# Kernel optimization log

Hardware: AMD Instinct MI355X
Metric: run time of the kernel (lower is better)

The kernel has to match this reference:

```python
import jax, jax.numpy as jnp
import numpy as np

SIM_COEFF = 25.0
COV_COEFF = 1.0
N, D = 32768, 512


def setup_inputs() -> dict:
    key = jax.random.key(0)
    k1, k2, k3 = jax.random.split(key, 3)
    z_a = jax.random.normal(k1, (N, D), dtype=jnp.float32)
    z_b = jax.random.normal(k2, (N, D), dtype=jnp.float32)
    # torch.randperm(N): values in [0, N) even though `combined` has 2N rows,
    # so both halves are drawn from z_a only (faithful to the original code).
    perm = jax.random.permutation(k3, N).astype(jnp.int32)
    return {"z_a": z_a, "z_b": z_b, "perm": perm}


def reference(z_a, z_b, perm):
    n, d = z_a.shape
    half = n // 2
    # repr (invariance) loss: MSE with mean reduction
    repr_loss = jnp.mean((z_a - z_b) ** 2)
    # combined has 2N rows but perm values < N -> selects rows of z_a
    combined = jnp.concatenate([z_a, z_b], axis=0)  # [2N, D]
    z1 = combined[perm[:half]]   # [N//2, D]
    z2 = combined[perm[half:]]   # [N - N//2, D]
    denom = jnp.float32(half - 1)  # original divides BOTH by N//2 - 1
    cov_z1 = (z1.T @ z1) / denom   # [D, D], replaces the per-sample outer-product loop
    cov_z2 = (z2.T @ z2) / denom   # [D, D]
    I = jnp.eye(d, dtype=z_a.dtype)
    cov_diff = (cov_z1 - I) @ (cov_z2 - I)
    cov_loss = jnp.sqrt(jnp.sum(cov_diff ** 2))  # Frobenius norm
    return SIM_COEFF * repr_loss + COV_COEFF * cov_loss
```

## Files before the change

kernel.cpp:

```cpp
#include <hip/hip_runtime.h>
#include <math.h>

typedef unsigned short u16;
typedef __attribute__((ext_vector_type(8))) short s16x8;
typedef __attribute__((ext_vector_type(4))) float f32x4;

#define NROWS 32768
#define DDIM 512
#define HALF 16384
#define KB 64
#define CSLICE 4
#define NSLICE 32
#define NSLOG2 5

__device__ __forceinline__ u16 f2bf(float f) {
  unsigned int u = __float_as_uint(f);
  unsigned int rounding = 0x7FFFu + ((u >> 16) & 1u);
  u += rounding;
  return (u16)(u >> 16);
}

__device__ __forceinline__ float bf2f(u16 h) {
  return __uint_as_float(((unsigned)h) << 16);
}

__device__ __forceinline__ float block_reduce(float v) {
  #pragma unroll
  for (int o = 32; o > 0; o >>= 1) v += __shfl_down(v, o);
  __shared__ float red[4];
  int w = threadIdx.x >> 6;
  if ((threadIdx.x & 63) == 0) red[w] = v;
  __syncthreads();
  return red[0] + red[1] + red[2] + red[3];
}

__global__ void inv_kernel(const int* __restrict__ perm, int* __restrict__ inv) {
  int i = blockIdx.x * 256 + threadIdx.x;
  inv[perm[i]] = i;
}

__device__ __forceinline__ float chunk_proc(float4 a0, float4 a1, float4 b0, float4 b1,
                                            int r, int c8, u16* z1, u16* z2) {
  uint4 o;
  o.x = (unsigned)f2bf(a0.x) | ((unsigned)f2bf(a0.y) << 16);
  o.y = (unsigned)f2bf(a0.z) | ((unsigned)f2bf(a0.w) << 16);
  o.z = (unsigned)f2bf(a1.x) | ((unsigned)f2bf(a1.y) << 16);
  o.w = (unsigned)f2bf(a1.z) | ((unsigned)f2bf(a1.w) << 16);
  u16* dst = (r < HALF) ? (z1 + (size_t)r * DDIM + c8) : (z2 + (size_t)(r - HALF) * DDIM + c8);
  *reinterpret_cast<uint4*>(dst) = o;
  float dx = a0.x - b0.x, dy = a0.y - b0.y, dz = a0.z - b0.z, dw = a0.w - b0.w;
  float ex = a1.x - b1.x, ey = a1.y - b1.y, ez = a1.z - b1.z, ew = a1.w - b1.w;
  return dx*dx + dy*dy + dz*dz + dw*dw + ex*ex + ey*ey + ez*ez + ew*ew;
}

__global__ __launch_bounds__(256) void scatter_repr_kernel(
    const float* __restrict__ za, const float* __restrict__ zb, const int* __restrict__ inv,
    u16* __restrict__ z1, u16* __restrict__ z2, float* __restrict__ psums) {
  int t = threadIdx.x;
  float acc = 0.0f;
  #pragma unroll
  for (int i = 0; i < 4; ++i) {
    int chunk = (i * 2048 + blockIdx.x) * 256 + t;
    int row = chunk >> 6;
    int c8 = (chunk & 63) << 3;
    const float4* pa = reinterpret_cast<const float4*>(za + (size_t)row * DDIM + c8);
    const float4* pb = reinterpret_cast<const float4*>(zb + (size_t)row * DDIM + c8);
    float4 a0 = pa[0], a1 = pa[1];
    float4 b0 = pb[0], b1 = pb[1];
    int r = inv[row];
    acc += chunk_proc(a0, a1, b0, b1, r, c8, z1, z2);
  }
  float tot = block_reduce(acc);
  if (t == 0) psums[blockIdx.x] = tot;
}

__device__ __forceinline__ int swz(int col) { return (((col >> 3) + col) & 7) << 3; }

__device__ __forceinline__ void store8(u16* lds, int c0, int kp, uint4 v0, uint4 v1) {
  const ushort* h0 = reinterpret_cast<const ushort*>(&v0);
  const ushort* h1 = reinterpret_cast<const ushort*>(&v1);
  #pragma unroll
  for (int j = 0; j < 8; ++j) {
    int col = c0 + j;
    unsigned w = (unsigned)h0[j] | ((unsigned)h1[j] << 16);
    *reinterpret_cast<unsigned*>(lds + col * KB + ((kp ^ swz(col)))) = w;
  }
}

__global__ __launch_bounds__(256) void gram_kernel(const u16* __restrict__ z1,
                                                   const u16* __restrict__ z2,
                                                   u16* __restrict__ parts) {
  int b = blockIdx.x;
  int mat = b & 1;
  int rest = b >> 1;
  int slice = rest & (NSLICE - 1);
  int tile = rest >> NSLOG2;
  int bi, bj;
  if (tile < 4)      { bi = 0; bj = tile; }
  else if (tile < 7) { bi = 1; bj = tile - 3; }
  else if (tile < 9) { bi = 2; bj = tile - 5; }
  else               { bi = 3; bj = 3; }
  int ti = bi * 128, tj = bj * 128;
  const u16* Z = mat ? z2 : z1;
  bool dual = (ti != tj);
  u16* P = parts + ((size_t)(mat * NSLICE + slice)) * (DDIM * DDIM);

  __shared__ u16 ldsA[128 * KB];
  __shared__ u16 ldsB[128 * KB];
  const u16* ldsBp = dual ? ldsB : ldsA;

  int t = threadIdx.x;
  int lane = t & 63;
  int wave = t >> 6;
  int wrow = (wave >> 1) * 64;
  int wcol = (wave & 1) * 64;
  int g = lane >> 4;
  int c = lane & 15;
  int h = lane >> 4;
  int c0 = (lane & 15) << 3;
  int kp0 = 8 * wave + 2 * h;

  f32x4 acc[4][4];
  #pragma unroll
  for (int m = 0; m < 4; ++m)
    #pragma unroll
    for (int n = 0; n < 4; ++n)
      #pragma unroll
      for (int r = 0; r < 4; ++r) acc[m][n][r] = 0.0f;

  uint4 xa0, xa1, xa2, xa3, xb0, xb1, xb2, xb3;
  uint4 ya0, ya1, ya2, ya3, yb0, yb1, yb2, yb3;

#define GLOAD(p, kkv) { \
    const u16* s0 = Z + (size_t)((kkv) + kp0) * DDIM; \
    const u16* s1 = Z + (size_t)((kkv) + kp0 + 32) * DDIM; \
    p##a0 = *reinterpret_cast<const uint4*>(s0 + ti + c0); \
    p##a1 = *reinterpret_cast<const uint4*>(s0 + DDIM + ti + c0); \
    p##a2 = *reinterpret_cast<const uint4*>(s1 + ti + c0); \
    p##a3 = *reinterpret_cast<const uint4*>(s1 + DDIM + ti + c0); \
    if (dual) { \
      p##b0 = *reinterpret_cast<const uint4*>(s0 + tj + c0); \
      p##b1 = *reinterpret_cast<const uint4*>(s0 + DDIM + tj + c0); \
      p##b2 = *reinterpret_cast<const uint4*>(s1 + tj + c0); \
      p##b3 = *reinterpret_cast<const uint4*>(s1 + DDIM + tj + c0); \
    } }

#define GSTORE(p) { \
    store8(ldsA, c0, kp0, p##a0, p##a1); \
    store8(ldsA, c0, kp0 + 32, p##a2, p##a3); \
    if (dual) { \
      store8(ldsB, c0, kp0, p##b0, p##b1); \
      store8(ldsB, c0, kp0 + 32, p##b2, p##b3); \
    } }

#define COMPUTE() { \
    _Pragma("unroll") \
    for (int ks = 0; ks < KB; ks += 32) { \
      s16x8 afr[4], bfr[4]; \
      _Pragma("unroll") \
      for (int m = 0; m < 4; ++m) { \
        int colA = wrow + m * 16 + c; \
        afr[m] = *reinterpret_cast<const s16x8*>(ldsA + colA * KB + ((ks + 8 * g) ^ swz(colA))); \
        int colB = wcol + m * 16 + c; \
        bfr[m] = *reinterpret_cast<const s16x8*>(ldsBp + colB * KB + ((ks + 8 * g) ^ swz(colB))); \
      } \
      _Pragma("unroll") \
      for (int m = 0; m < 4; ++m) \
        _Pragma("unroll") \
        for (int n = 0; n < 4; ++n) \
          acc[m][n] = __builtin_amdgcn_mfma_f32_16x16x32_bf16(afr[m], bfr[n], acc[m][n], 0, 0, 0); \
    } }

  const int kspan = HALF >> NSLOG2;
  const int k0 = slice * kspan;
  GLOAD(x, k0);
  for (int kk = k0; kk < k0 + kspan; kk += 2 * KB) {
    __syncthreads();
    GSTORE(x);
    __syncthreads();
    GLOAD(y, kk + KB);
    COMPUTE();
    __syncthreads();
    GSTORE(y);
    __syncthreads();
    if (kk + 2 * KB < k0 + kspan) GLOAD(x, kk + 2 * KB);
    COMPUTE();
  }
#undef GLOAD
#undef GSTORE
#undef COMPUTE

  #pragma unroll
  for (int m = 0; m < 4; ++m)
    #pragma unroll
    for (int n = 0; n < 4; ++n)
      #pragma unroll
      for (int r = 0; r < 4; ++r) {
        int orow = ti + wrow + m * 16 + 4 * g + r;
        int ocol = tj + wcol + n * 16 + c;
        P[orow * DDIM + ocol] = f2bf(acc[m][n][r]);
      }
}

__global__ void reduce_parts_kernel(const u16* __restrict__ parts, float* __restrict__ cov) {
  int idx = blockIdx.x * 256 + threadIdx.x;
  int mat = (idx >= 40960) ? 1 : 0;
  int tl = idx - mat * 40960;
  int region = tl >> 12;
  int o = tl & 4095;
  int bi, bj;
  if (region < 4)      { bi = 0; bj = region; }
  else if (region < 7) { bi = 1; bj = region - 3; }
  else if (region < 9) { bi = 2; bj = region - 5; }
  else                 { bi = 3; bj = 3; }
  int r = bi * 128 + (o >> 5);
  int cc = bj * 128 + ((o & 31) << 2);
  const u16* base = parts + (size_t)mat * NSLICE * (DDIM * DDIM);
  float sx = 0.f, sy = 0.f, sz = 0.f, sw = 0.f;
  #pragma unroll 4
  for (int j = 0; j < NSLICE; ++j) {
    ushort4 v = *reinterpret_cast<const ushort4*>(base + (size_t)j * (DDIM * DDIM) + r * DDIM + cc);
    sx += bf2f(v.x); sy += bf2f(v.y); sz += bf2f(v.z); sw += bf2f(v.w);
  }
  const float inv = 1.0f / 16383.0f;
  sx *= inv; sy *= inv; sz *= inv; sw *= inv;
  float* cv = cov + (size_t)mat * (DDIM * DDIM);
  float4 ov; ov.x = sx; ov.y = sy; ov.z = sz; ov.w = sw;
  *reinterpret_cast<float4*>(cv + r * DDIM + cc) = ov;
  if (bi != bj) {
    cv[(cc + 0) * DDIM + r] = sx;
    cv[(cc + 1) * DDIM + r] = sy;
    cv[(cc + 2) * DDIM + r] = sz;
    cv[(cc + 3) * DDIM + r] = sw;
  }
}

__global__ __launch_bounds__(256) void covdiff_part_kernel(const float* __restrict__ cov,
                                                           float* __restrict__ pcov) {
  int bid = blockIdx.x;
  int bx = bid & 15, by = (bid >> 4) & 15, sl = bid >> 8;
  int r0 = by * 32, c0 = bx * 32, ks = sl * 128;
  const float* c1 = cov;
  const float* c2 = cov + DDIM * DDIM;
  __shared__ float ldsA[32 * 132];
  __shared__ float ldsB[128 * 33];
  int t = threadIdx.x;
  #pragma unroll
  for (int j = 0; j < 4; ++j) {
    int f4 = t + 256 * j;
    int row = f4 >> 5;
    int k4 = (f4 & 31) << 2;
    float4 v = *reinterpret_cast<const float4*>(c1 + (size_t)(r0 + row) * DDIM + ks + k4);
    int gr = r0 + row;
    if (gr == ks + k4 + 0) v.x -= 1.f;
    if (gr == ks + k4 + 1) v.y -= 1.f;
    if (gr == ks + k4 + 2) v.z -= 1.f;
    if (gr == ks + k4 + 3) v.w -= 1.f;
    *reinterpret_cast<float4*>(&ldsA[row * 132 + k4]) = v;
  }
  {
    int c = t & 31;
    int kb = t >> 5;
    #pragma unroll
    for (int j = 0; j < 16; ++j) {
      int k = kb + 8 * j;
      float v = c2[(size_t)(ks + k) * DDIM + c0 + c];
      if (ks + k == c0 + c) v -= 1.f;
      ldsB[k * 33 + c] = v;
    }
  }
  __syncthreads();
  int col = t & 31;
  int ty = t >> 5;
  float e0 = 0.f, e1 = 0.f, e2 = 0.f, e3 = 0.f;
  #pragma unroll 4
  for (int k = 0; k < 128; ++k) {
    float bv = ldsB[k * 33 + col];
    e0 = fmaf(ldsA[(ty * 4 + 0) * 132 + k], bv, e0);
    e1 = fmaf(ldsA[(ty * 4 + 1) * 132 + k], bv, e1);
    e2 = fmaf(ldsA[(ty * 4 + 2) * 132 + k], bv, e2);
    e3 = fmaf(ldsA[(ty * 4 + 3) * 132 + k], bv, e3);
  }
  float* P = pcov + (size_t)sl * (DDIM * DDIM);
  P[(r0 + ty * 4 + 0) * DDIM + c0 + col] = e0;
  P[(r0 + ty * 4 + 1) * DDIM + c0 + col] = e1;
  P[(r0 + ty * 4 + 2) * DDIM + c0 + col] = e2;
  P[(r0 + ty * 4 + 3) * DDIM + c0 + col] = e3;
}

__global__ void covred_kernel(const float* __restrict__ pcov, float* __restrict__ psums2) {
  int idx = blockIdx.x * 256 + threadIdx.x;
  float sx = 0.f, sy = 0.f, sz = 0.f, sw = 0.f;
  #pragma unroll
  for (int j = 0; j < CSLICE; ++j) {
    float4 v = reinterpret_cast<const float4*>(pcov)[idx + j * 65536];
    sx += v.x; sy += v.y; sz += v.z; sw += v.w;
  }
  float q = sx * sx + sy * sy + sz * sz + sw * sw;
  float tot = block_reduce(q);
  if (threadIdx.x == 0) psums2[blockIdx.x] = tot;
}

__global__ void finalize_kernel(const float* __restrict__ psums,
                                const float* __restrict__ psums2,
                                float* __restrict__ out) {
  int t = threadIdx.x;
  float a = 0.f;
  #pragma unroll
  for (int j = 0; j < 8; ++j) a += psums[t + 256 * j];
  float b = psums2[t];
  float ta = block_reduce(a);
  __syncthreads();
  float tb = block_reduce(b);
  if (t == 0) out[0] = 25.0f * (ta / 16777216.0f) + sqrtf(tb);
}

extern "C" void kernel_launch(void* const* d_in, const int* in_sizes, int n_in,
                              void* d_out, int out_size, void* d_ws, size_t ws_size,
                              hipStream_t stream) {
  const float* za = (const float*)d_in[0];
  const float* zb = (const float*)d_in[1];
  const int* perm = (const int*)d_in[2];
  float* out = (float*)d_out;
  char* ws = (char*)d_ws;

  float* psums = (float*)ws;
  float* psums2 = (float*)(ws + 8192);
  size_t off = 16384;
  u16* parts = (u16*)(ws + off);
  off += (size_t)2 * NSLICE * DDIM * DDIM * 2;
  float* cov = (float*)(ws + off);
  off += (size_t)2 * DDIM * DDIM * 4;
  u16* z1 = (u16*)(ws + off);
  u16* z2 = z1 + (size_t)HALF * DDIM;
  float* pcov = (float*)z1;
  off += (size_t)2 * HALF * DDIM * 2;
  int* inv = (int*)(ws + off);

  inv_kernel<<<NROWS / 256, 256, 0, stream>>>(perm, inv);
  scatter_repr_kernel<<<2048, 256, 0, stream>>>(za, zb, inv, z1, z2, psums);
  gram_kernel<<<2 * 10 * NSLICE, 256, 0, stream>>>(z1, z2, parts);
  reduce_parts_kernel<<<320, 256, 0, stream>>>(parts, cov);
  covdiff_part_kernel<<<16 * 16 * CSLICE, 256, 0, stream>>>(cov, pcov);
  covred_kernel<<<256, 256, 0, stream>>>(pcov, psums2);
  finalize_kernel<<<1, 256, 0, stream>>>(psums, psums2, out);
}
```

Measured before the change: 78.96 us.

## Accumulate Gram split-K partials with fp32 atomics instead of bf16 slice buffers

The Gram kernel now adds its per-slice partial results straight into a zeroed fp32 buffer with atomicAdd, instead of writing 32 bf16 partial matrices that a later kernel had to read back and sum. The reduce kernel becomes a simple scale-and-mirror fixup, and a memset is added to clear the accumulator. This removes about 32 MB of partial writes and reads, at the cost of atomic contention on 32 slices per element and an extra memset. The scatter kernel also gets twice as many blocks, each doing half the work, with the final reduction widened to match.

```diff
diff --git a/kernel.cpp b/kernel.cpp
--- a/kernel.cpp
+++ b/kernel.cpp
@@ -18,10 +18,6 @@
   unsigned int rounding = 0x7FFFu + ((u >> 16) & 1u);
   u += rounding;
   return (u16)(u >> 16);
-}
-
-__device__ __forceinline__ float bf2f(u16 h) {
-  return __uint_as_float(((unsigned)h) << 16);
 }
 
 __device__ __forceinline__ float block_reduce(float v) {
@@ -59,8 +55,8 @@
   int t = threadIdx.x;
   float acc = 0.0f;
   #pragma unroll
-  for (int i = 0; i < 4; ++i) {
-    int chunk = (i * 2048 + blockIdx.x) * 256 + t;
+  for (int i = 0; i < 2; ++i) {
+    int chunk = (i * 4096 + blockIdx.x) * 256 + t;
     int row = chunk >> 6;
     int c8 = (chunk & 63) << 3;
     const float4* pa = reinterpret_cast<const float4*>(za + (size_t)row * DDIM + c8);
@@ -89,7 +85,7 @@
 
 __global__ __launch_bounds__(256) void gram_kernel(const u16* __restrict__ z1,
                                                    const u16* __restrict__ z2,
-                                                   u16* __restrict__ parts) {
+                                                   float* __restrict__ rawG) {
   int b = blockIdx.x;
   int mat = b & 1;
   int rest = b >> 1;
@@ -103,7 +99,7 @@
   int ti = bi * 128, tj = bj * 128;
   const u16* Z = mat ? z2 : z1;
   bool dual = (ti != tj);
-  u16* P = parts + ((size_t)(mat * NSLICE + slice)) * (DDIM * DDIM);
+  float* G = rawG + (size_t)mat * (DDIM * DDIM);
 
   __shared__ u16 ldsA[128 * KB];
   __shared__ u16 ldsB[128 * KB];
@@ -198,11 +194,11 @@
       for (int r = 0; r < 4; ++r) {
         int orow = ti + wrow + m * 16 + 4 * g + r;
         int ocol = tj + wcol + n * 16 + c;
-        P[orow * DDIM + ocol] = f2bf(acc[m][n][r]);
+        atomicAdd(&G[orow * DDIM + ocol], acc[m][n][r]);
       }
 }
 
-__global__ void reduce_parts_kernel(const u16* __restrict__ parts, float* __restrict__ cov) {
+__global__ void fixup_kernel(const float* __restrict__ rawG, float* __restrict__ cov) {
   int idx = blockIdx.x * 256 + threadIdx.x;
   int mat = (idx >= 40960) ? 1 : 0;
   int tl = idx - mat * 40960;
@@ -215,23 +211,17 @@
   else                 { bi = 3; bj = 3; }
   int r = bi * 128 + (o >> 5);
   int cc = bj * 128 + ((o & 31) << 2);
-  const u16* base = parts + (size_t)mat * NSLICE * (DDIM * DDIM);
-  float sx = 0.f, sy = 0.f, sz = 0.f, sw = 0.f;
-  #pragma unroll 4
-  for (int j = 0; j < NSLICE; ++j) {
-    ushort4 v = *reinterpret_cast<const ushort4*>(base + (size_t)j * (DDIM * DDIM) + r * DDIM + cc);
-    sx += bf2f(v.x); sy += bf2f(v.y); sz += bf2f(v.z); sw += bf2f(v.w);
-  }
+  size_t pos = (size_t)r * DDIM + cc;
+  float4 v = *reinterpret_cast<const float4*>(rawG + (size_t)mat * (DDIM * DDIM) + pos);
   const float inv = 1.0f / 16383.0f;
-  sx *= inv; sy *= inv; sz *= inv; sw *= inv;
+  v.x *= inv; v.y *= inv; v.z *= inv; v.w *= inv;
   float* cv = cov + (size_t)mat * (DDIM * DDIM);
-  float4 ov; ov.x = sx; ov.y = sy; ov.z = sz; ov.w = sw;
-  *reinterpret_cast<float4*>(cv + r * DDIM + cc) = ov;
+  *reinterpret_cast<float4*>(cv + pos) = v;
   if (bi != bj) {
-    cv[(cc + 0) * DDIM + r] = sx;
-    cv[(cc + 1) * DDIM + r] = sy;
-    cv[(cc + 2) * DDIM + r] = sz;
-    cv[(cc + 3) * DDIM + r] = sw;
+    cv[(cc + 0) * DDIM + r] = v.x;
+    cv[(cc + 1) * DDIM + r] = v.y;
+    cv[(cc + 2) * DDIM + r] = v.z;
+    cv[(cc + 3) * DDIM + r] = v.w;
   }
 }
 
@@ -307,7 +297,7 @@
   int t = threadIdx.x;
   float a = 0.f;
   #pragma unroll
-  for (int j = 0; j < 8; ++j) a += psums[t + 256 * j];
+  for (int j = 0; j < 16; ++j) a += psums[t + 256 * j];
   float b = psums2[t];
   float ta = block_reduce(a);
   __syncthreads();
@@ -325,10 +315,11 @@
   char* ws = (char*)d_ws;
 
   float* psums = (float*)ws;
-  float* psums2 = (float*)(ws + 8192);
-  size_t off = 16384;
-  u16* parts = (u16*)(ws + off);
-  off += (size_t)2 * NSLICE * DDIM * DDIM * 2;
+  float* psums2 = (float*)(ws + 16384);
+  size_t off = 20480;
+  float* rawG = (float*)(ws + off);
+  size_t rawBytes = (size_t)2 * DDIM * DDIM * 4;
+  off += rawBytes;
   float* cov = (float*)(ws + off);
   off += (size_t)2 * DDIM * DDIM * 4;
   u16* z1 = (u16*)(ws + off);
@@ -337,10 +328,11 @@
   off += (size_t)2 * HALF * DDIM * 2;
   int* inv = (int*)(ws + off);
 
+  (void)hipMemsetAsync(rawG, 0, rawBytes, stream);
   inv_kernel<<<NROWS / 256, 256, 0, stream>>>(perm, inv);
-  scatter_repr_kernel<<<2048, 256, 0, stream>>>(za, zb, inv, z1, z2, psums);
-  gram_kernel<<<2 * 10 * NSLICE, 256, 0, stream>>>(z1, z2, parts);
-  reduce_parts_kernel<<<320, 256, 0, stream>>>(parts, cov);
+  scatter_repr_kernel<<<4096, 256, 0, stream>>>(za, zb, inv, z1, z2, psums);
+  gram_kernel<<<2 * 10 * NSLICE, 256, 0, stream>>>(z1, z2, rawG);
+  fixup_kernel<<<320, 256, 0, stream>>>(rawG, cov);
   covdiff_part_kernel<<<16 * 16 * CSLICE, 256, 0, stream>>>(cov, pcov);
   covred_kernel<<<256, 256, 0, stream>>>(pcov, psums2);
   finalize_kernel<<<1, 256, 0, stream>>>(psums, psums2, out);
```

Result: slower. 106.2 us (+34.4%).

## Fuse permutation gather and bf16 conversion into the Gram kernel

Applied to the files above, without the earlier changes.

Drops the inverse-permutation and scatter kernels that wrote permuted bf16 copies of z_a into the workspace. The Gram kernel now stages its 512-row slice of perm in LDS, gathers fp32 rows of z_a directly, and packs them to bf16 before storing to LDS. The repr loss becomes a plain streaming kernel over z_a and z_b. This removes a full write and re-read of the bf16 intermediate plus one launch, at the cost of the Gram kernel reading fp32 rows by scattered index and holding twice as many prefetch registers.

```diff
diff --git a/kernel.cpp b/kernel.cpp
--- a/kernel.cpp
+++ b/kernel.cpp
@@ -13,11 +13,11 @@
 #define NSLICE 32
 #define NSLOG2 5
 
-__device__ __forceinline__ u16 f2bf(float f) {
+__device__ __forceinline__ unsigned f2bf(float f) {
   unsigned int u = __float_as_uint(f);
   unsigned int rounding = 0x7FFFu + ((u >> 16) & 1u);
   u += rounding;
-  return (u16)(u >> 16);
+  return u >> 16;
 }
 
 __device__ __forceinline__ float bf2f(u16 h) {
@@ -34,44 +34,21 @@
   return red[0] + red[1] + red[2] + red[3];
 }
 
-__global__ void inv_kernel(const int* __restrict__ perm, int* __restrict__ inv) {
-  int i = blockIdx.x * 256 + threadIdx.x;
-  inv[perm[i]] = i;
-}
-
-__device__ __forceinline__ float chunk_proc(float4 a0, float4 a1, float4 b0, float4 b1,
-                                            int r, int c8, u16* z1, u16* z2) {
-  uint4 o;
-  o.x = (unsigned)f2bf(a0.x) | ((unsigned)f2bf(a0.y) << 16);
-  o.y = (unsigned)f2bf(a0.z) | ((unsigned)f2bf(a0.w) << 16);
-  o.z = (unsigned)f2bf(a1.x) | ((unsigned)f2bf(a1.y) << 16);
-  o.w = (unsigned)f2bf(a1.z) | ((unsigned)f2bf(a1.w) << 16);
-  u16* dst = (r < HALF) ? (z1 + (size_t)r * DDIM + c8) : (z2 + (size_t)(r - HALF) * DDIM + c8);
-  *reinterpret_cast<uint4*>(dst) = o;
-  float dx = a0.x - b0.x, dy = a0.y - b0.y, dz = a0.z - b0.z, dw = a0.w - b0.w;
-  float ex = a1.x - b1.x, ey = a1.y - b1.y, ez = a1.z - b1.z, ew = a1.w - b1.w;
-  return dx*dx + dy*dy + dz*dz + dw*dw + ex*ex + ey*ey + ez*ez + ew*ew;
-}
-
-__global__ __launch_bounds__(256) void scatter_repr_kernel(
-    const float* __restrict__ za, const float* __restrict__ zb, const int* __restrict__ inv,
-    u16* __restrict__ z1, u16* __restrict__ z2, float* __restrict__ psums) {
-  int t = threadIdx.x;
+__global__ __launch_bounds__(256) void repr_kernel(
+    const float* __restrict__ za, const float* __restrict__ zb, float* __restrict__ psums) {
+  int tid = blockIdx.x * 256 + threadIdx.x;
+  const int S = 524288;
   float acc = 0.0f;
   #pragma unroll
-  for (int i = 0; i < 4; ++i) {
-    int chunk = (i * 2048 + blockIdx.x) * 256 + t;
-    int row = chunk >> 6;
-    int c8 = (chunk & 63) << 3;
-    const float4* pa = reinterpret_cast<const float4*>(za + (size_t)row * DDIM + c8);
-    const float4* pb = reinterpret_cast<const float4*>(zb + (size_t)row * DDIM + c8);
-    float4 a0 = pa[0], a1 = pa[1];
-    float4 b0 = pb[0], b1 = pb[1];
-    int r = inv[row];
-    acc += chunk_proc(a0, a1, b0, b1, r, c8, z1, z2);
+  for (int i = 0; i < 8; ++i) {
+    size_t idx = (size_t)(i * S + tid);
+    float4 a = reinterpret_cast<const float4*>(za)[idx];
+    float4 b = reinterpret_cast<const float4*>(zb)[idx];
+    float dx = a.x - b.x, dy = a.y - b.y, dz = a.z - b.z, dw = a.w - b.w;
+    acc += dx * dx + dy * dy + dz * dz + dw * dw;
   }
   float tot = block_reduce(acc);
-  if (t == 0) psums[blockIdx.x] = tot;
+  if (threadIdx.x == 0) psums[blockIdx.x] = tot;
 }
 
 __device__ __forceinline__ int swz(int col) { return (((col >> 3) + col) & 7) << 3; }
@@ -87,8 +64,17 @@
   }
 }
 
-__global__ __launch_bounds__(256) void gram_kernel(const u16* __restrict__ z1,
-                                                   const u16* __restrict__ z2,
+__device__ __forceinline__ uint4 pack8(float4 x, float4 y) {
+  uint4 o;
+  o.x = f2bf(x.x) | (f2bf(x.y) << 16);
+  o.y = f2bf(x.z) | (f2bf(x.w) << 16);
+  o.z = f2bf(y.x) | (f2bf(y.y) << 16);
+  o.w = f2bf(y.z) | (f2bf(y.w) << 16);
+  return o;
+}
+
+__global__ __launch_bounds__(256) void gram_kernel(const float* __restrict__ za,
+                                                   const int* __restrict__ perm,
                                                    u16* __restrict__ parts) {
   int b = blockIdx.x;
   int mat = b & 1;
@@ -101,12 +87,12 @@
   else if (tile < 9) { bi = 2; bj = tile - 5; }
   else               { bi = 3; bj = 3; }
   int ti = bi * 128, tj = bj * 128;
-  const u16* Z = mat ? z2 : z1;
   bool dual = (ti != tj);
   u16* P = parts + ((size_t)(mat * NSLICE + slice)) * (DDIM * DDIM);
 
   __shared__ u16 ldsA[128 * KB];
   __shared__ u16 ldsB[128 * KB];
+  __shared__ int plds[512];
   const u16* ldsBp = dual ? ldsB : ldsA;
 
   int t = threadIdx.x;
@@ -120,6 +106,11 @@
   int c0 = (lane & 15) << 3;
   int kp0 = 8 * wave + 2 * h;
 
+  int pbase = mat * HALF + slice * 512;
+  plds[t] = perm[pbase + t];
+  plds[t + 256] = perm[pbase + t + 256];
+  __syncthreads();
+
   f32x4 acc[4][4];
   #pragma unroll
   for (int m = 0; m < 4; ++m)
@@ -128,29 +119,43 @@
       #pragma unroll
       for (int r = 0; r < 4; ++r) acc[m][n][r] = 0.0f;
 
-  uint4 xa0, xa1, xa2, xa3, xb0, xb1, xb2, xb3;
-  uint4 ya0, ya1, ya2, ya3, yb0, yb1, yb2, yb3;
+  float4 xa0, xa1, xa2, xa3, xa4, xa5, xa6, xa7;
+  float4 xb0, xb1, xb2, xb3, xb4, xb5, xb6, xb7;
+  float4 ya0, ya1, ya2, ya3, ya4, ya5, ya6, ya7;
+  float4 yb0, yb1, yb2, yb3, yb4, yb5, yb6, yb7;
 
 #define GLOAD(p, kkv) { \
-    const u16* s0 = Z + (size_t)((kkv) + kp0) * DDIM; \
-    const u16* s1 = Z + (size_t)((kkv) + kp0 + 32) * DDIM; \
-    p##a0 = *reinterpret_cast<const uint4*>(s0 + ti + c0); \
-    p##a1 = *reinterpret_cast<const uint4*>(s0 + DDIM + ti + c0); \
-    p##a2 = *reinterpret_cast<const uint4*>(s1 + ti + c0); \
-    p##a3 = *reinterpret_cast<const uint4*>(s1 + DDIM + ti + c0); \
+    int r0 = plds[(kkv) + kp0], r1 = plds[(kkv) + kp0 + 1]; \
+    int r2 = plds[(kkv) + kp0 + 32], r3 = plds[(kkv) + kp0 + 33]; \
+    const float* q0 = za + (size_t)r0 * DDIM; \
+    const float* q1 = za + (size_t)r1 * DDIM; \
+    const float* q2 = za + (size_t)r2 * DDIM; \
+    const float* q3 = za + (size_t)r3 * DDIM; \
+    p##a0 = *reinterpret_cast<const float4*>(q0 + ti + c0); \
+    p##a1 = *reinterpret_cast<const float4*>(q0 + ti + c0 + 4); \
+    p##a2 = *reinterpret_cast<const float4*>(q1 + ti + c0); \
+    p##a3 = *reinterpret_cast<const float4*>(q1 + ti + c0 + 4); \
+    p##a4 = *reinterpret_cast<const float4*>(q2 + ti + c0); \
+    p##a5 = *reinterpret_cast<const float4*>(q2 + ti + c0 + 4); \
+    p##a6 = *reinterpret_cast<const float4*>(q3 + ti + c0); \
+    p##a7 = *reinterpret_cast<const float4*>(q3 + ti + c0 + 4); \
     if (dual) { \
-      p##b0 = *reinterpret_cast<const uint4*>(s0 + tj + c0); \
-      p##b1 = *reinterpret_cast<const uint4*>(s0 + DDIM + tj + c0); \
-      p##b2 = *reinterpret_cast<const uint4*>(s1 + tj + c0); \
-      p##b3 = *reinterpret_cast<const uint4*>(s1 + DDIM + tj + c0); \
+      p##b0 = *reinterpret_cast<const float4*>(q0 + tj + c0); \
+      p##b1 = *reinterpret_cast<const float4*>(q0 + tj + c0 + 4); \
+      p##b2 = *reinterpret_cast<const float4*>(q1 + tj + c0); \
+      p##b3 = *reinterpret_cast<const float4*>(q1 + tj + c0 + 4); \
+      p##b4 = *reinterpret_cast<const float4*>(q2 + tj + c0); \
+      p##b5 = *reinterpret_cast<const float4*>(q2 + tj + c0 + 4); \
+      p##b6 = *reinterpret_cast<const float4*>(q3 + tj + c0); \
+      p##b7 = *reinterpret_cast<const float4*>(q3 + tj + c0 + 4); \
     } }
 
 #define GSTORE(p) { \
-    store8(ldsA, c0, kp0, p##a0, p##a1); \
-    store8(ldsA, c0, kp0 + 32, p##a2, p##a3); \
+    store8(ldsA, c0, kp0, pack8(p##a0, p##a1), pack8(p##a2, p##a3)); \
+    store8(ldsA, c0, kp0 + 32, pack8(p##a4, p##a5), pack8(p##a6, p##a7)); \
     if (dual) { \
-      store8(ldsB, c0, kp0, p##b0, p##b1); \
-      store8(ldsB, c0, kp0 + 32, p##b2, p##b3); \
+      store8(ldsB, c0, kp0, pack8(p##b0, p##b1), pack8(p##b2, p##b3)); \
+      store8(ldsB, c0, kp0 + 32, pack8(p##b4, p##b5), pack8(p##b6, p##b7)); \
     } }
 
 #define COMPUTE() { \
@@ -171,10 +176,8 @@
           acc[m][n] = __builtin_amdgcn_mfma_f32_16x16x32_bf16(afr[m], bfr[n], acc[m][n], 0, 0, 0); \
     } }
 
-  const int kspan = HALF >> NSLOG2;
-  const int k0 = slice * kspan;
-  GLOAD(x, k0);
-  for (int kk = k0; kk < k0 + kspan; kk += 2 * KB) {
+  GLOAD(x, 0);
+  for (int kk = 0; kk < 512; kk += 2 * KB) {
     __syncthreads();
     GSTORE(x);
     __syncthreads();
@@ -183,7 +186,7 @@
     __syncthreads();
     GSTORE(y);
     __syncthreads();
-    if (kk + 2 * KB < k0 + kspan) GLOAD(x, kk + 2 * KB);
+    if (kk + 2 * KB < 512) GLOAD(x, kk + 2 * KB);
     COMPUTE();
   }
 #undef GLOAD
@@ -198,7 +201,7 @@
       for (int r = 0; r < 4; ++r) {
         int orow = ti + wrow + m * 16 + 4 * g + r;
         int ocol = tj + wcol + n * 16 + c;
-        P[orow * DDIM + ocol] = f2bf(acc[m][n][r]);
+        P[orow * DDIM + ocol] = (u16)f2bf(acc[m][n][r]);
       }
 }
 
@@ -327,19 +330,13 @@
   float* psums = (float*)ws;
   float* psums2 = (float*)(ws + 8192);
   size_t off = 16384;
-  u16* parts = (u16*)(ws + off);
-  off += (size_t)2 * NSLICE * DDIM * DDIM * 2;
   float* cov = (float*)(ws + off);
   off += (size_t)2 * DDIM * DDIM * 4;
-  u16* z1 = (u16*)(ws + off);
-  u16* z2 = z1 + (size_t)HALF * DDIM;
-  float* pcov = (float*)z1;
-  off += (size_t)2 * HALF * DDIM * 2;
-  int* inv = (int*)(ws + off);
-
-  inv_kernel<<<NROWS / 256, 256, 0, stream>>>(perm, inv);
-  scatter_repr_kernel<<<2048, 256, 0, stream>>>(za, zb, inv, z1, z2, psums);
-  gram_kernel<<<2 * 10 * NSLICE, 256, 0, stream>>>(z1, z2, parts);
+  u16* parts = (u16*)(ws + off);
+  float* pcov = (float*)parts;
+
+  repr_kernel<<<2048, 256, 0, stream>>>(za, zb, psums);
+  gram_kernel<<<2 * 10 * NSLICE, 256, 0, stream>>>(za, perm, parts);
   reduce_parts_kernel<<<320, 256, 0, stream>>>(parts, cov);
   covdiff_part_kernel<<<16 * 16 * CSLICE, 256, 0, stream>>>(cov, pcov);
   covred_kernel<<<256, 256, 0, stream>>>(pcov, psums2);
```

Result: slower. 86.84 us (+10.0%).
